# Kernel optimization log

Hardware: AMD Instinct MI355X
Metric: run time of the kernel (lower is better)

## Reference

```python
import jax, jax.numpy as jnp
import numpy as np
from jax import lax

# Static config matching init_kwargs
CIN, COUT, K, STRIDE, PAD = 64, 64, 3, 1, 1
SCALE = 100.0          # scale_factor
MIN_SUMMARY = -512     # static lower bound for the quantized-summary memo table
MEM_SIZE = 1025        # static memo table size (covers summaries in [-512, 512])


def setup_inputs() -> dict:
    key = jax.random.key(0)
    k1, k2, k3 = jax.random.split(key, 3)
    fmap = jax.random.normal(k1, (8, CIN, 112, 112), dtype=jnp.float32)
    weight = jax.random.normal(k2, (COUT, K * K * CIN), dtype=jnp.float32) * 0.05
    bias = jax.random.normal(k3, (COUT,), dtype=jnp.float32) * 0.05
    return {"fmap": fmap, "weight": weight, "bias": bias}


def _unfold(fmap):
    # torch F.unfold(fmap, K, stride, pad).permute(0,2,1): [N, P, K*K*Cin]
    patches = lax.conv_general_dilated_patches(
        fmap, (K, K), (STRIDE, STRIDE), ((PAD, PAD), (PAD, PAD)))  # [N, Cin*K*K, Hout, Wout]
    N, D, Hout, Wout = patches.shape
    return patches.reshape(N, D, Hout * Wout).transpose(0, 2, 1), Hout, Wout


def reference(fmap, weight, bias):
    patches, Hout, Wout = _unfold(fmap)          # [N, P, D]
    N, P, D = patches.shape

    # Quantized avg summary per patch: fmap.mean(dim=2).mul_(scale).int()
    summaries = (patches.mean(axis=2) * SCALE).astype(jnp.int32)  # [N, P]
    bins = jnp.clip(summaries - MIN_SUMMARY, 0, MEM_SIZE - 1)     # [N, P]

    def per_image(p, b):
        # Dedup: each summary bin computed once from its first-occurring patch.
        idx = jnp.arange(P, dtype=jnp.int32)
        first = jnp.full((MEM_SIZE,), P, dtype=jnp.int32).at[b].min(idx)  # scatter-min
        rep_patch = p[first[b]]                   # [P, D] gather of representatives
        return rep_patch @ weight.T + bias        # [P, Cout]

    out = jax.vmap(per_image)(patches, bins)      # [N, P, Cout]
    return out.transpose(0, 2, 1).reshape(N, COUT, Hout, Wout)


if __name__ == "__main__":
    inp = setup_inputs()
    print(reference(**inp).shape)
```

## Files before the change

### kernel.cpp

```cpp
#include <hip/hip_runtime.h>

#define N_IMG 8
#define CIN   64
#define H     112
#define W     112
#define P     (H * W)
#define PG    (P / 4)
#define D     576
#define COUT  64
#define MEM   1025
#define RB    4
#define NBAND (H / RB)
#define HALO_PIX ((RB + 2) * W)
#define OUT_PIX  (RB * W)
#define NB_BINS (N_IMG * NBAND)
#define NB_WT   16

__global__ __launch_bounds__(256) void fused_bins_kernel(
    const float* __restrict__ fmap, const float* __restrict__ weight,
    float* __restrict__ wT, int* __restrict__ bins,
    unsigned* __restrict__ first) {
  __shared__ double Tl[HALO_PIX];
  __shared__ int lfirst[MEM];
  const int t = threadIdx.x;
  const int g = blockIdx.x;

  if (g >= NB_BINS) {
    for (int i = (g - NB_BINS) * 256 + t; i < D * COUT; i += NB_WT * 256) {
      int co = i / D, d = i - co * D;
      wT[d * COUT + co] = weight[i];
    }
    return;
  }

  const int n = g / NBAND;
  const int band = g - n * NBAND;
  const int r0 = band * RB;

  for (int i = t; i < MEM; i += 256) lfirst[i] = P;

  const float* fb = fmap + (size_t)n * CIN * P;
  for (int j = t; j < HALO_PIX; j += 256) {
    int lr = j / W, w = j - lr * W;
    int gh = r0 - 1 + lr;
    double s = 0.0;
    if (gh >= 0 && gh < H) {
      const float* pp = fb + gh * W + w;
      #pragma unroll
      for (int c = 0; c < CIN; ++c) s += (double)pp[(size_t)c * P];
    }
    Tl[j] = s;
  }
  __syncthreads();

  for (int k = t; k < OUT_PIX; k += 256) {
    int orow = k / W, w = k - orow * W;
    double s = 0.0;
    #pragma unroll
    for (int dh = 0; dh < 3; ++dh) {
      const double* row = &Tl[(orow + dh) * W];
      #pragma unroll
      for (int dw = -1; dw <= 1; ++dw) {
        int ww = w + dw;
        if (ww < 0 || ww >= W) continue;
        s += row[ww];
      }
    }
    float sf = (float)s;
    float mean = sf / 576.0f;
    float v = mean * 100.0f;
    int qv = (int)v;
    int b = qv + 512;
    b = b < 0 ? 0 : (b > MEM - 1 ? MEM - 1 : b);
    int p = (r0 + orow) * W + w;
    bins[n * P + p] = b;
    atomicMin(&lfirst[b], p);
  }
  __syncthreads();

  for (int i = t; i < MEM; i += 256) {
    int v = lfirst[i];
    if (v != P) atomicMin(&first[n * MEM + i], (unsigned)v);
  }
}

__global__ __launch_bounds__(256) void rep_kernel(
    const float* __restrict__ fmap, const float* __restrict__ wT,
    const float* __restrict__ bias, const unsigned* __restrict__ first,
    float* __restrict__ rep) {
  const int pair = blockIdx.x;
  unsigned fi = first[pair];
  if (fi >= (unsigned)P) return;
  const int n = pair / MEM;
  __shared__ float patch[D];
  __shared__ float partial[4][COUT];
  const int t = threadIdx.x;
  int h = (int)fi / W, w = (int)fi - h * W;
  for (int d = t; d < D; d += 256) {
    int c = d / 9, r = d - c * 9;
    int kh = r / 3, kw = r - kh * 3;
    int hh = h + kh - 1, ww = w + kw - 1;
    float val = 0.0f;
    if (hh >= 0 && hh < H && ww >= 0 && ww < W)
      val = fmap[((size_t)(n * CIN + c)) * P + hh * W + ww];
    patch[d] = val;
  }
  __syncthreads();
  int co = t & 63, seg = t >> 6;
  float acc = 0.0f;
  int d0 = seg * 144;
  #pragma unroll 4
  for (int d = d0; d < d0 + 144; ++d)
    acc += patch[d] * wT[d * COUT + co];
  partial[seg][co] = acc;
  __syncthreads();
  if (t < COUT) {
    float total = partial[0][t] + partial[1][t] + partial[2][t] + partial[3][t] + bias[t];
    rep[((size_t)pair) * COUT + t] = total;
  }
}

__global__ __launch_bounds__(256) void scatter_kernel(
    const int* __restrict__ bins, const float* __restrict__ rep,
    float* __restrict__ out) {
  int idx = blockIdx.x * 256 + threadIdx.x;
  if (idx >= N_IMG * COUT * PG) return;
  int pv = idx % PG;
  int rest = idx / PG;
  int co = rest & 63;
  int n = rest >> 6;
  int4 b4 = *reinterpret_cast<const int4*>(bins + n * P + pv * 4);
  const float* repn = rep + (size_t)n * MEM * COUT + co;
  float4 o;
  o.x = repn[(size_t)b4.x * COUT];
  o.y = repn[(size_t)b4.y * COUT];
  o.z = repn[(size_t)b4.z * COUT];
  o.w = repn[(size_t)b4.w * COUT];
  *reinterpret_cast<float4*>(out + ((size_t)n * COUT + co) * P + pv * 4) = o;
}

extern "C" void kernel_launch(void* const* d_in, const int* in_sizes, int n_in,
                              void* d_out, int out_size, void* d_ws, size_t ws_size,
                              hipStream_t stream) {
  const float* fmap   = (const float*)d_in[0];
  const float* weight = (const float*)d_in[1];
  const float* bias   = (const float*)d_in[2];
  float* out = (float*)d_out;

  char* ws = (char*)d_ws;
  int*      bins  = (int*)     (ws);
  unsigned* first = (unsigned*)(ws + 401408);
  float*    wT    = (float*)   (ws + 434240);
  float*    rep   = (float*)   (ws + 581696);

  hipMemsetAsync(first, 0xFF, N_IMG * MEM * sizeof(unsigned), stream);

  hipLaunchKernelGGL(fused_bins_kernel, dim3(NB_BINS + NB_WT), dim3(256), 0, stream,
                     fmap, weight, wT, bins, first);
  hipLaunchKernelGGL(rep_kernel, dim3(N_IMG * MEM), dim3(256), 0, stream,
                     fmap, wT, bias, first, rep);
  hipLaunchKernelGGL(scatter_kernel, dim3((N_IMG * COUT * PG + 255) / 256), dim3(256), 0, stream,
                     bins, rep, out);
}
```

Baseline: 113.8 us.

## Drop memset and global atomics via per-band first tables; vectorize channel sums

The per-image first-occurrence table is no longer built with global atomicMin after a memset. Each band block now writes its own full local table, and rep_kernel reduces across the 14 bands when it reads them. Band height doubles to 8 rows, which cuts halo recomputation, and the channel-sum loop reads float4 vectors. The cost is more rep_kernel reads per block (14 loads per pair) and fewer bin blocks (112), which lowers parallelism in the first kernel.

After: 116.2 us. +2.0%, slower.

```diff
diff --git a/kernel.cpp b/kernel.cpp
--- a/kernel.cpp
+++ b/kernel.cpp
@@ -9,17 +9,19 @@
 #define D     576
 #define COUT  64
 #define MEM   1025
-#define RB    4
+#define RB    8
 #define NBAND (H / RB)
-#define HALO_PIX ((RB + 2) * W)
-#define OUT_PIX  (RB * W)
+#define HALO_ROWS (RB + 2)
+#define HALO_PIX  (HALO_ROWS * W)
+#define HALO_F4   (HALO_PIX / 4)
+#define OUT_PIX   (RB * W)
 #define NB_BINS (N_IMG * NBAND)
 #define NB_WT   16
 
 __global__ __launch_bounds__(256) void fused_bins_kernel(
     const float* __restrict__ fmap, const float* __restrict__ weight,
     float* __restrict__ wT, int* __restrict__ bins,
-    unsigned* __restrict__ first) {
+    int* __restrict__ first_band) {
   __shared__ double Tl[HALO_PIX];
   __shared__ int lfirst[MEM];
   const int t = threadIdx.x;
@@ -40,16 +42,21 @@
   for (int i = t; i < MEM; i += 256) lfirst[i] = P;
 
   const float* fb = fmap + (size_t)n * CIN * P;
-  for (int j = t; j < HALO_PIX; j += 256) {
-    int lr = j / W, w = j - lr * W;
+  for (int u = t; u < HALO_F4; u += 256) {
+    int lr = u / (W / 4);
+    int wu = u - lr * (W / 4);
     int gh = r0 - 1 + lr;
-    double s = 0.0;
+    double s0 = 0.0, s1 = 0.0, s2 = 0.0, s3 = 0.0;
     if (gh >= 0 && gh < H) {
-      const float* pp = fb + gh * W + w;
+      const float* pp = fb + gh * W + wu * 4;
       #pragma unroll
-      for (int c = 0; c < CIN; ++c) s += (double)pp[(size_t)c * P];
+      for (int c = 0; c < CIN; ++c) {
+        float4 v = *reinterpret_cast<const float4*>(pp + (size_t)c * P);
+        s0 += (double)v.x; s1 += (double)v.y; s2 += (double)v.z; s3 += (double)v.w;
+      }
     }
-    Tl[j] = s;
+    double* dst = &Tl[lr * W + wu * 4];
+    dst[0] = s0; dst[1] = s1; dst[2] = s2; dst[3] = s3;
   }
   __syncthreads();
 
@@ -78,24 +85,29 @@
   }
   __syncthreads();
 
-  for (int i = t; i < MEM; i += 256) {
-    int v = lfirst[i];
-    if (v != P) atomicMin(&first[n * MEM + i], (unsigned)v);
-  }
+  int* dst = first_band + ((size_t)n * NBAND + band) * MEM;
+  for (int i = t; i < MEM; i += 256) dst[i] = lfirst[i];
 }
 
 __global__ __launch_bounds__(256) void rep_kernel(
     const float* __restrict__ fmap, const float* __restrict__ wT,
-    const float* __restrict__ bias, const unsigned* __restrict__ first,
+    const float* __restrict__ bias, const int* __restrict__ first_band,
     float* __restrict__ rep) {
   const int pair = blockIdx.x;
-  unsigned fi = first[pair];
-  if (fi >= (unsigned)P) return;
   const int n = pair / MEM;
+  const int b = pair - n * MEM;
+  const int* fbp = first_band + (size_t)n * NBAND * MEM + b;
+  int fi = P;
+  #pragma unroll
+  for (int band = 0; band < NBAND; ++band) {
+    int v = fbp[(size_t)band * MEM];
+    fi = v < fi ? v : fi;
+  }
+  if (fi >= P) return;
   __shared__ float patch[D];
   __shared__ float partial[4][COUT];
   const int t = threadIdx.x;
-  int h = (int)fi / W, w = (int)fi - h * W;
+  int h = fi / W, w = fi - h * W;
   for (int d = t; d < D; d += 256) {
     int c = d / 9, r = d - c * 9;
     int kh = r / 3, kw = r - kh * 3;
@@ -148,17 +160,15 @@
   float* out = (float*)d_out;
 
   char* ws = (char*)d_ws;
-  int*      bins  = (int*)     (ws);
-  unsigned* first = (unsigned*)(ws + 401408);
-  float*    wT    = (float*)   (ws + 434240);
-  float*    rep   = (float*)   (ws + 581696);
-
-  hipMemsetAsync(first, 0xFF, N_IMG * MEM * sizeof(unsigned), stream);
+  int*   bins       = (int*)  (ws);
+  int*   first_band = (int*)  (ws + 401408);
+  float* wT         = (float*)(ws + 860608);
+  float* rep        = (float*)(ws + 1008064);
 
   hipLaunchKernelGGL(fused_bins_kernel, dim3(NB_BINS + NB_WT), dim3(256), 0, stream,
-                     fmap, weight, wT, bins, first);
+                     fmap, weight, wT, bins, first_band);
   hipLaunchKernelGGL(rep_kernel, dim3(N_IMG * MEM), dim3(256), 0, stream,
-                     fmap, wT, bias, first, rep);
+                     fmap, wT, bias, first_band, rep);
   hipLaunchKernelGGL(scatter_kernel, dim3((N_IMG * COUT * PG + 255) / 256), dim3(256), 0, stream,
                      bins, rep, out);
 }
```
